# Kernel tuning notes

Hardware: AMD Instinct MI355X
Metric: run time of the kernel (lower is better)

## Reference

```python
import jax, jax.numpy as jnp
import numpy as np

NUM_WORDS = 32768
MAX_CHARS = 20
NUM_CHARS = 128
EMB = 64
H = 128   # word_hidden_size (per direction)
C = 128   # context_vector_size


def setup_inputs() -> dict:
    key = jax.random.key(0)
    ks = jax.random.split(key, 16)
    s = 1.0 / np.sqrt(H)  # torch GRU default init scale
    u = lambda k, shape, sc: jax.random.uniform(k, shape, jnp.float32, -sc, sc)
    inp = {
        'padded_char_tensor': jax.random.randint(ks[0], (NUM_WORDS, MAX_CHARS), 0, NUM_CHARS),
        'sequence_lens': jax.random.randint(ks[1], (NUM_WORDS,), 1, MAX_CHARS + 1),
        'emb': jax.random.normal(ks[2], (NUM_CHARS, EMB), jnp.float32),
        # forward-direction GRU params (torch layout: gates r,z,n stacked)
        'Wih_f': u(ks[3], (3 * H, EMB), s),
        'Whh_f': u(ks[4], (3 * H, H), s),
        'bih_f': u(ks[5], (3 * H,), s),
        'bhh_f': u(ks[6], (3 * H,), s),
        # backward-direction GRU params
        'Wih_b': u(ks[7], (3 * H, EMB), s),
        'Whh_b': u(ks[8], (3 * H, H), s),
        'bih_b': u(ks[9], (3 * H,), s),
        'bhh_b': u(ks[10], (3 * H,), s),
        # word_projection Linear(2H -> C)
        'Wp': u(ks[11], (C, 2 * H), 1.0 / np.sqrt(2 * H)),
        'bp': u(ks[12], (C,), 1.0 / np.sqrt(2 * H)),
        # word context vector [C, 1]
        'ctx': u(ks[13], (C, 1), 0.1),
    }
    return inp


def _gru_dir(x_proj, Whh, bhh):
    # x_proj: [B, T, 3H] precomputed input projection; scan over T
    Hn = Whh.shape[1]
    def step(h, xt):
        hp = h @ Whh.T + bhh
        r = jax.nn.sigmoid(xt[:, :Hn] + hp[:, :Hn])
        z = jax.nn.sigmoid(xt[:, Hn:2 * Hn] + hp[:, Hn:2 * Hn])
        n = jnp.tanh(xt[:, 2 * Hn:] + r * hp[:, 2 * Hn:])
        h = (1.0 - z) * n + z * h
        return h, h
    h0 = jnp.zeros((x_proj.shape[0], Hn), x_proj.dtype)
    _, ys = jax.lax.scan(step, h0, x_proj.transpose(1, 0, 2))
    return ys.transpose(1, 0, 2)  # [B, T, H]


def _rev_within(x, lens):
    # reverse each sequence within its valid length (packed-sequence semantics)
    T = x.shape[1]
    t = jnp.arange(T)[None, :]
    idx = jnp.where(t < lens[:, None], lens[:, None] - 1 - t, t)
    return jnp.take_along_axis(x, idx[:, :, None], axis=1)


def _forward(chars, lens, emb, Wih_f, Whh_f, bih_f, bhh_f,
             Wih_b, Whh_b, bih_b, bhh_b, Wp, bp, ctx):
    x = emb[chars]  # [B, T, EMB]; dropout_p=0 -> identity
    mask = (jnp.arange(x.shape[1])[None, :] < lens[:, None])  # [B, T]
    out_f = _gru_dir(x @ Wih_f.T + bih_f, Whh_f, bhh_f)
    xb = _rev_within(x, lens)
    out_b = _gru_dir(xb @ Wih_b.T + bih_b, Whh_b, bhh_b)
    out_b = _rev_within(out_b, lens)
    # pad_packed_sequence zero-pads beyond each length
    out = jnp.concatenate([out_f, out_b], axis=-1) * mask[:, :, None]  # [B, T, 2H]
    proj = jnp.tanh(out @ Wp.T + bp)                # [B, T, C]
    scores = jnp.einsum('btc,c->bt', proj, ctx[:, 0])
    att = jax.nn.softmax(scores, axis=-1)           # softmax over char positions
    return jnp.einsum('bt,btd->bd', att, out)       # [B, 2H]


def reference(padded_char_tensor, sequence_lens, emb, Wih_f, Whh_f, bih_f, bhh_f,
              Wih_b, Whh_b, bih_b, bhh_b, Wp, bp, ctx):
    return _forward(padded_char_tensor, sequence_lens, emb, Wih_f, Whh_f, bih_f,
                    bhh_f, Wih_b, Whh_b, bih_b, bhh_b, Wp, bp, ctx)
```

## Files before the change

### kernel.cpp

```cpp
#include <hip/hip_runtime.h>
#include <hip/hip_bf16.h>
#include <stdint.h>


typedef unsigned short u16;
typedef float f32x4 __attribute__((ext_vector_type(4)));
typedef __bf16 bf16x8 __attribute__((ext_vector_type(8)));

#if __has_builtin(__builtin_amdgcn_exp2f)
#define EXP2F(x) __builtin_amdgcn_exp2f(x)
#else
#define EXP2F(x) exp2f(x)
#endif
#if __has_builtin(__builtin_amdgcn_rcpf)
#define RCPF(x) __builtin_amdgcn_rcpf(x)
#else
#define RCPF(x) (1.0f / (x))
#endif

#define LOG2E 1.4426950408889634f

__device__ __forceinline__ u16 f2b(float f) {
  uint32_t u = __builtin_bit_cast(uint32_t, f);
  u = u + 0x7FFFu + ((u >> 16) & 1u);
  return (u16)(u >> 16);
}
__device__ __forceinline__ float b2f(u16 s) {
  uint32_t u = ((uint32_t)s) << 16;
  return __builtin_bit_cast(float, u);
}
__device__ __forceinline__ float fast_tanh(float x) {
  return 1.0f - 2.0f * RCPF(EXP2F(2.0f * LOG2E * x) + 1.0f);
}
__device__ __forceinline__ uint32_t cvtpk(float a, float b) {
  uint32_t r;
  asm("v_cvt_pk_bf16_f32 %0, %1, %2" : "=v"(r) : "v"(a), "v"(b));
  return r;
}

__global__ void prep_kernel(
    const float* __restrict__ emb,
    const float* __restrict__ wih_f, const float* __restrict__ bih_f,
    const float* __restrict__ wih_b, const float* __restrict__ bih_b,
    const float* __restrict__ bhh_f, const float* __restrict__ bhh_b,
    const float* __restrict__ whh_f_in, const float* __restrict__ whh_b_in,
    const float* __restrict__ wp_in,
    float* __restrict__ xpf_f, float* __restrict__ xpf_b,
    u16* __restrict__ whhf, u16* __restrict__ whhb, u16* __restrict__ wpf) {
  int gid = blockIdx.x * 256 + threadIdx.x;
  if (blockIdx.x < 384) {
    int e = gid;
    int d = (e >= 49152) ? 1 : 0;
    int r = e - d * 49152;
    int j = r & 3;
    int e2 = r >> 2;
    int cls = e2 % 3;
    int e3 = e2 / 3;
    int grp = e3 & 3;
    int e4 = e3 >> 2;
    int wv = e4 & 7;
    int c = e4 >> 3;
    int row = cls * 128 + wv * 16 + grp * 4 + j;
    const float* wih = d ? wih_b : wih_f;
    const float* bih = d ? bih_b : bih_f;
    const float* bhh = d ? bhh_b : bhh_f;
    const float4* e4p = (const float4*)(emb + c * 64);
    const float4* w4p = (const float4*)(wih + row * 64);
    float s = 0.f;
#pragma unroll
    for (int q = 0; q < 16; q++) {
      float4 a = e4p[q], b = w4p[q];
      s += a.x * b.x + a.y * b.y + a.z * b.z + a.w * b.w;
    }
    s += bih[row];
    float scale;
    if (cls < 2) {
      s += bhh[row];
      scale = -LOG2E;
    } else {
      scale = 2.0f * LOG2E;
    }
    (d ? xpf_b : xpf_f)[r] = s * scale;
  } else if (blockIdx.x < 432) {
    int idx = gid - 384 * 256;
    int d = (idx >= 6144) ? 1 : 0;
    int r = idx - d * 6144;
    int lane = r & 63, kt = (r >> 6) & 3, nt = r >> 8;
    float scale = (nt < 16) ? -LOG2E : 2.0f * LOG2E;
    int n = nt * 16 + (lane & 15);
    int k0 = kt * 32 + (lane >> 4) * 8;
    const float* w = d ? whh_b_in : whh_f_in;
    u16* o = (d ? whhb : whhf) + r * 8;
    for (int j = 0; j < 8; j++) o[j] = f2b(w[n * 128 + k0 + j] * scale);
  } else {
    int idx = gid - 432 * 256;
    if (idx < 4096) {
      int lane = idx & 63, kt = (idx >> 6) & 7, nt = idx >> 9;
      int n = nt * 16 + (lane & 15);
      int k0 = kt * 32 + (lane >> 4) * 8;
      u16* o = wpf + idx * 8;
      for (int j = 0; j < 8; j++) o[j] = f2b(wp_in[n * 256 + k0 + j]);
    }
  }
}

__global__ void sort_zero(int* __restrict__ bins) {
  if (threadIdx.x < 32) bins[threadIdx.x] = 0;
}
__global__ void sort_hist(const int* __restrict__ lens, int* __restrict__ bins) {
  __shared__ int hcnt[32];
  int tid = threadIdx.x;
  if (tid < 32) hcnt[tid] = 0;
  __syncthreads();
  int gid = blockIdx.x * 256 + tid;
  int l = lens[gid] & 31;
  atomicAdd(&hcnt[l], 1);
  __syncthreads();
  if (tid < 32 && hcnt[tid]) atomicAdd(&bins[tid], hcnt[tid]);
}
__global__ void sort_scan(const int* __restrict__ bins, int* __restrict__ offsw,
                          const float* __restrict__ bp,
                          const float* __restrict__ ctx,
                          float* __restrict__ c0out) {
  if (threadIdx.x == 0 && blockIdx.x == 0) {
    int off = 0;
    for (int l = 0; l < 32; l++) {
      offsw[l] = off;
      off += bins[l];
    }
    float c0 = 0.f;
    for (int c = 0; c < 128; c++) c0 += fast_tanh(bp[c]) * ctx[c];
    *c0out = c0;
  }
}
__global__ void sort_scat(const int* __restrict__ lens, int* __restrict__ offsw,
                          int* __restrict__ perm) {
  __shared__ int lcnt[32];
  __shared__ int lbase[32];
  int tid = threadIdx.x;
  if (tid < 32) lcnt[tid] = 0;
  __syncthreads();
  int gid = blockIdx.x * 256 + tid;
  int l = lens[gid] & 31;
  int lr = atomicAdd(&lcnt[l], 1);
  __syncthreads();
  if (tid < 32) lbase[tid] = lcnt[tid] ? atomicAdd(&offsw[tid], lcnt[tid]) : 0;
  __syncthreads();
  perm[lbase[l] + lr] = gid;
}

__global__ __launch_bounds__(512, 4) void gru_kernel(
    const int* __restrict__ chars, const int* __restrict__ lens,
    const int* __restrict__ perm,
    const float* __restrict__ xpf_f, const float* __restrict__ xpf_b,
    const u16* __restrict__ whhf, const u16* __restrict__ whhb,
    const float* __restrict__ bhh_f, const float* __restrict__ bhh_b,
    u16* __restrict__ hf, u16* __restrict__ hb, int word_off, int nbd) {
  const int bid = blockIdx.x;
  const int dir = bid & 1;
  const int wg = nbd - 1 - (bid >> 1);
  const int tid = threadIdx.x;

  __shared__ int perm_s[16];
  __shared__ unsigned char lens_s[16];
  __shared__ int coff_s[320];
  __shared__ u16 h_s[2][2048];

  if (tid < 16) {
    int p = perm[word_off + wg * 16 + tid];
    perm_s[tid] = p;
    lens_s[tid] = (unsigned char)lens[p];
  }
  for (int i = tid; i < 1024; i += 512) ((uint32_t*)h_s)[i] = 0u;
  __syncthreads();
  for (int i = tid; i < 320; i += 512) {
    int w = i & 15, s = i >> 4;
    int L = lens_s[w];
    int t = dir ? ((s < L) ? (L - 1 - s) : s) : s;
    coff_s[s * 16 + w] = chars[perm_s[w] * 20 + t] * 384;
  }

  const float* xp = dir ? xpf_b : xpf_f;
  const u16* whh = dir ? whhb : whhf;
  const float* bhh = dir ? bhh_b : bhh_f;
  u16* hout = (dir ? hb : hf) + (size_t)wg * 16 * 2560;

  const int wv = tid >> 6, ln = tid & 63, word = ln & 15, grp = ln >> 4;
  const float* xpt = xp + (wv * 4 + grp) * 12;

  bf16x8 Wf[3][4];
#pragma unroll
  for (int cls = 0; cls < 3; cls++) {
    int nt = cls * 8 + wv;
#pragma unroll
    for (int kt = 0; kt < 4; kt++)
      Wf[cls][kt] = *(const bf16x8*)(whh + (((nt * 4 + kt) * 64 + ln) << 3));
  }
  float4 bhn = *(const float4*)(bhh + 256 + wv * 16 + grp * 4);
  bhn.x *= 2.0f * LOG2E; bhn.y *= 2.0f * LOG2E;
  bhn.z *= 2.0f * LOG2E; bhn.w *= 2.0f * LOG2E;

  __syncthreads();

  const int Lmax = lens_s[15];

  const int hw_off =
      (((wv >> 1) * 64) + (word | (((wv & 1) * 2 + (grp >> 1)) << 4))) * 16 +
      (grp & 1) * 8;
  const int swd = tid >> 5;
  const int k4 = (tid & 31) << 2;
  const int sL = lens_s[swd];
  const int hs_off =
      (((k4 >> 5) * 64) + (swd | (((k4 >> 3) & 3) << 4))) * 16 + (k4 & 7) * 2;

  char* hsb = (char*)h_s;

  float hreg[4] = {0.f, 0.f, 0.f, 0.f};
  f32x4 xA0, xA1, xA2, xB0, xB1, xB2;
  {
    int off = coff_s[word];
    xA0 = *(const f32x4*)(xpt + off);
    xA1 = *(const f32x4*)(xpt + off + 4);
    xA2 = *(const f32x4*)(xpt + off + 8);
  }

#define GSTEP(S, PAR, XC0, XC1, XC2, XN0, XN1, XN2)                           \
  {                                                                           \
    if ((S) + 1 < Lmax) {                                                     \
      int off = coff_s[((S) + 1) * 16 + word];                                \
      XN0 = *(const f32x4*)(xpt + off);                                       \
      XN1 = *(const f32x4*)(xpt + off + 4);                                   \
      XN2 = *(const f32x4*)(xpt + off + 8);                                   \
    }                                                                         \
    f32x4 a0 = (f32x4){0.f, 0.f, 0.f, 0.f};                                   \
    f32x4 a1 = (f32x4){0.f, 0.f, 0.f, 0.f};                                   \
    f32x4 a2 = (f32x4){bhn.x, bhn.y, bhn.z, bhn.w};                           \
    _Pragma("unroll")                                                         \
    for (int kt = 0; kt < 4; kt++) {                                          \
      bf16x8 Hf =                                                             \
          *(const bf16x8*)(hsb + (PAR) * 4096 + ((kt * 64 + ln) << 4));       \
      a0 = __builtin_amdgcn_mfma_f32_16x16x32_bf16(Wf[0][kt], Hf, a0, 0, 0, 0); \
      a1 = __builtin_amdgcn_mfma_f32_16x16x32_bf16(Wf[1][kt], Hf, a1, 0, 0, 0); \
      a2 = __builtin_amdgcn_mfma_f32_16x16x32_bf16(Wf[2][kt], Hf, a2, 0, 0, 0); \
    }                                                                         \
    _Pragma("unroll")                                                         \
    for (int r = 0; r < 4; r++) {                                             \
      float rr = RCPF(1.0f + EXP2F(XC0[r] + a0[r]));                          \
      float zz = RCPF(1.0f + EXP2F(XC1[r] + a1[r]));                          \
      float na = fmaf(rr, a2[r], XC2[r]);                                     \
      float nn = fmaf(-2.0f, RCPF(EXP2F(na) + 1.0f), 1.0f);                   \
      hreg[r] = fmaf(zz, hreg[r] - nn, nn);                                   \
    }                                                                         \
    {                                                                         \
      uint2 pk = make_uint2(cvtpk(hreg[0], hreg[1]), cvtpk(hreg[2], hreg[3]));\
      *(uint2*)(hsb + ((PAR) ^ 1) * 4096 + hw_off) = pk;                      \
    }                                                                         \
    __syncthreads();                                                          \
    if ((S) < sL) {                                                           \
      int tdst = dir ? (sL - 1 - (S)) : (S);                                  \
      uint2 v = *(const uint2*)(hsb + ((PAR) ^ 1) * 4096 + hs_off);           \
      *(uint2*)(hout + ((size_t)swd * 20 + tdst) * 128 + k4) = v;             \
    }                                                                         \
  }

  for (int s = 0; s < Lmax; s += 2) {
    GSTEP(s, 0, xA0, xA1, xA2, xB0, xB1, xB2);
    if (s + 1 < Lmax) GSTEP(s + 1, 1, xB0, xB1, xB2, xA0, xA1, xA2);
  }
#undef GSTEP
}

__global__ __launch_bounds__(256, 2) void attn_kernel(
    const u16* __restrict__ hf, const u16* __restrict__ hb,
    const u16* __restrict__ wpf,
    const float* __restrict__ bp, const float* __restrict__ ctx,
    const int* __restrict__ perm, const int* __restrict__ lens,
    const float* __restrict__ c0p,
    float* __restrict__ out, int word_off) {
  const int blk = gridDim.x - 1 - blockIdx.x;
  const int lw0 = blk * 16;

  __shared__ u16 ot_s[4096];
  __shared__ float part_s[4][16];
  __shared__ int perm_s[16];
  __shared__ unsigned char lens_s[16];

  const int tid = threadIdx.x;
  const int wv = tid >> 6, ln = tid & 63, col = ln & 15, grp = ln >> 4;
  const int sw = tid >> 4;
  const int seg = tid & 15;

  if (tid < 16) {
    int p = perm[word_off + lw0 + tid];
    perm_s[tid] = p;
    lens_s[tid] = (unsigned char)lens[p];
  }
  __syncthreads();
  const int Lmax = lens_s[15];
  const int Lw = lens_s[sw];

  float bpv[2], ctxv[2];
#pragma unroll
  for (int n = 0; n < 2; n++) {
    int nt = wv + n * 4;
    bpv[n] = bp[nt * 16 + col];
    ctxv[n] = ctx[nt * 16 + col];
  }

  float facc[16];
#pragma unroll
  for (int i = 0; i < 16; i++) facc[i] = 0.f;
  float mrun = -3.0e38f, drun = 0.f;

  const u16* srcbase =
      ((seg < 8) ? hf : hb) + (size_t)(lw0 + sw) * 2560 + (seg & 7) * 16;

  uint4 vn[2];
#pragma unroll
  for (int q = 0; q < 2; q++) vn[q] = *(const uint4*)(srcbase + q * 8);

  for (int t = 0; t < Lmax; t++) {
    uint4 v[2];
    v[0] = vn[0];
    v[1] = vn[1];

#pragma unroll
    for (int q = 0; q < 2; q++) {
      int idx = seg * 2 + q;
      int kt = idx >> 2;
      int lane_a = sw | ((idx & 3) << 4);
      *(uint4*)(ot_s + ((kt * 64 + lane_a) << 3)) = v[q];
    }
    if (t + 1 < Lmax) {
      const u16* src = srcbase + (t + 1) * 128;
#pragma unroll
      for (int q = 0; q < 2; q++) vn[q] = *(const uint4*)(src + q * 8);
    }
    __syncthreads();

    f32x4 acc[2];
#pragma unroll
    for (int n = 0; n < 2; n++) acc[n] = (f32x4){bpv[n], bpv[n], bpv[n], bpv[n]};

#pragma unroll
    for (int kt = 0; kt < 8; kt++) {
      bf16x8 Af = *(const bf16x8*)(ot_s + ((kt * 64 + ln) << 3));
#pragma unroll
      for (int n = 0; n < 2; n++) {
        int nt = wv + n * 4;
        bf16x8 Bf = *(const bf16x8*)(wpf + (((nt * 8 + kt) * 64 + ln) << 3));
        acc[n] = __builtin_amdgcn_mfma_f32_16x16x32_bf16(Af, Bf, acc[n], 0, 0, 0);
      }
    }

#pragma unroll
    for (int r = 0; r < 4; r++) {
      float p = fast_tanh(acc[0][r]) * ctxv[0] + fast_tanh(acc[1][r]) * ctxv[1];
      p += __shfl_xor(p, 1, 64);
      p += __shfl_xor(p, 2, 64);
      p += __shfl_xor(p, 4, 64);
      p += __shfl_xor(p, 8, 64);
      if (col == 0) part_s[wv][grp * 4 + r] = p;
    }
    __syncthreads();

    float sc = part_s[0][sw] + part_s[1][sw] + part_s[2][sw] + part_s[3][sw];

    if (t < Lw) {
      float mnew = fmaxf(mrun, sc);
      float scale = EXP2F(LOG2E * (mrun - mnew));
      float e = EXP2F(LOG2E * (sc - mnew));
      drun = drun * scale + e;
      mrun = mnew;
#pragma unroll
      for (int q = 0; q < 2; q++) {
        const u16* pv = (const u16*)&v[q];
#pragma unroll
        for (int j = 0; j < 8; j++)
          facc[q * 8 + j] = facc[q * 8 + j] * scale + e * b2f(pv[j]);
      }
    }
  }

  drun += (float)(20 - Lw) * EXP2F(LOG2E * (*c0p - mrun));

  float inv = RCPF(drun);
  float* dst = out + (size_t)perm_s[sw] * 256 + seg * 16;
#pragma unroll
  for (int i = 0; i < 4; i++) {
    float4 o = make_float4(facc[i * 4] * inv, facc[i * 4 + 1] * inv,
                           facc[i * 4 + 2] * inv, facc[i * 4 + 3] * inv);
    *(float4*)(dst + i * 4) = o;
  }
}

extern "C" void kernel_launch(void* const* d_in, const int* in_sizes, int n_in,
                              void* d_out, int out_size, void* d_ws, size_t ws_size,
                              hipStream_t stream) {
  const int* chars = (const int*)d_in[0];
  const int* lens = (const int*)d_in[1];
  const float* emb = (const float*)d_in[2];
  const float* wih_f = (const float*)d_in[3];
  const float* whh_f = (const float*)d_in[4];
  const float* bih_f = (const float*)d_in[5];
  const float* bhh_f = (const float*)d_in[6];
  const float* wih_b = (const float*)d_in[7];
  const float* whh_b = (const float*)d_in[8];
  const float* bih_b = (const float*)d_in[9];
  const float* bhh_b = (const float*)d_in[10];
  const float* wp = (const float*)d_in[11];
  const float* bp = (const float*)d_in[12];
  const float* ctx = (const float*)d_in[13];
  float* outp = (float*)d_out;

  uint8_t* ws = (uint8_t*)d_ws;
  float* xpf_f = (float*)(ws + 0);
  float* xpf_b = (float*)(ws + 196608);
  u16* whhf = (u16*)(ws + 393216);
  u16* whhb = (u16*)(ws + 491520);
  u16* wpf = (u16*)(ws + 589824);
  int* bins = (int*)(ws + 655360);
  int* offsw = (int*)(ws + 655488);
  float* c0p = (float*)(ws + 655616);
  int* permp = (int*)(ws + 655680);
  const size_t H_OFF = 1048576;

  prep_kernel<<<448, 256, 0, stream>>>(emb, wih_f, bih_f, wih_b, bih_b, bhh_f,
                                       bhh_b, whh_f, whh_b, wp, xpf_f, xpf_b,
                                       whhf, whhb, wpf);
  sort_zero<<<1, 64, 0, stream>>>(bins);
  sort_hist<<<128, 256, 0, stream>>>(lens, bins);
  sort_scan<<<1, 64, 0, stream>>>(bins, offsw, bp, ctx, c0p);
  sort_scat<<<128, 256, 0, stream>>>(lens, offsw, permp);

  const size_t per_word = 20 * 128 * 2 * 2;
  size_t avail = (ws_size > H_OFF) ? (ws_size - H_OFF) : 0;
  int maxw = (int)(avail / per_word) & ~63;
  if (maxw > 32768) maxw = 32768;
  if (maxw < 64) maxw = 64;

  for (int done = 0; done < 32768;) {
    int nw = (32768 - done < maxw) ? (32768 - done) : maxw;
    u16* hfp = (u16*)(ws + H_OFF);
    u16* hbp = hfp + (size_t)nw * 2560;
    int nbd = nw / 16;
    gru_kernel<<<2 * nbd, 512, 0, stream>>>(chars, lens, permp, xpf_f, xpf_b,
                                            whhf, whhb, bhh_f, bhh_b, hfp, hbp,
                                            done, nbd);
    attn_kernel<<<nw / 16, 256, 0, stream>>>(hfp, hbp, wpf, bp, ctx, permp,
                                             lens, c0p, outp, done);
    done += nw;
  }
}
```

Before: 276.3 us.

## Process two 16-word groups per GRU block to interleave independent recurrences

Each GRU workgroup now handles 32 words as two independent 16-word sub-batches, issuing MFMA chains for both before the gate math so the two recurrences can hide each other's latency and share one barrier per step. Register-resident Whh weights are reused across twice as many words and the grid is halved. The cross-step prefetch of input projections is dropped in favour of loading at the start of each step. Risks include higher register pressure under the 512x4 launch bounds, fewer blocks to fill the GPU, and a loop bound set by the longest of 32 words.

```diff
diff --git a/kernel.cpp b/kernel.cpp
--- a/kernel.cpp
+++ b/kernel.cpp
@@ -161,29 +161,29 @@
   const int wg = nbd - 1 - (bid >> 1);
   const int tid = threadIdx.x;
 
-  __shared__ int perm_s[16];
-  __shared__ unsigned char lens_s[16];
-  __shared__ int coff_s[320];
-  __shared__ u16 h_s[2][2048];
-
-  if (tid < 16) {
-    int p = perm[word_off + wg * 16 + tid];
+  __shared__ int perm_s[32];
+  __shared__ unsigned char lens_s[32];
+  __shared__ int coff_s[640];
+  __shared__ u16 h_s[2][2][2048];
+
+  if (tid < 32) {
+    int p = perm[word_off + wg * 32 + tid];
     perm_s[tid] = p;
     lens_s[tid] = (unsigned char)lens[p];
   }
-  for (int i = tid; i < 1024; i += 512) ((uint32_t*)h_s)[i] = 0u;
-  __syncthreads();
-  for (int i = tid; i < 320; i += 512) {
-    int w = i & 15, s = i >> 4;
+  for (int i = tid; i < 4096; i += 512) ((uint32_t*)h_s)[i] = 0u;
+  __syncthreads();
+  for (int i = tid; i < 640; i += 512) {
+    int w = i & 31, s = i >> 5;
     int L = lens_s[w];
     int t = dir ? ((s < L) ? (L - 1 - s) : s) : s;
-    coff_s[s * 16 + w] = chars[perm_s[w] * 20 + t] * 384;
+    coff_s[s * 32 + w] = chars[perm_s[w] * 20 + t] * 384;
   }
 
   const float* xp = dir ? xpf_b : xpf_f;
   const u16* whh = dir ? whhb : whhf;
   const float* bhh = dir ? bhh_b : bhh_f;
-  u16* hout = (dir ? hb : hf) + (size_t)wg * 16 * 2560;
+  u16* hout = (dir ? hb : hf) + (size_t)wg * 32 * 2560;
 
   const int wv = tid >> 6, ln = tid & 63, word = ln & 15, grp = ln >> 4;
   const float* xpt = xp + (wv * 4 + grp) * 12;
@@ -202,36 +202,31 @@
 
   __syncthreads();
 
-  const int Lmax = lens_s[15];
+  const int Lmax = lens_s[31];
 
   const int hw_off =
       (((wv >> 1) * 64) + (word | (((wv & 1) * 2 + (grp >> 1)) << 4))) * 16 +
       (grp & 1) * 8;
   const int swd = tid >> 5;
   const int k4 = (tid & 31) << 2;
-  const int sL = lens_s[swd];
+  const int sLA = lens_s[swd];
+  const int sLB = lens_s[16 + swd];
   const int hs_off =
       (((k4 >> 5) * 64) + (swd | (((k4 >> 3) & 3) << 4))) * 16 + (k4 & 7) * 2;
+  u16* houtA = hout + (size_t)swd * 2560 + k4;
+  u16* houtB = hout + (size_t)(16 + swd) * 2560 + k4;
 
   char* hsb = (char*)h_s;
 
-  float hreg[4] = {0.f, 0.f, 0.f, 0.f};
-  f32x4 xA0, xA1, xA2, xB0, xB1, xB2;
-  {
-    int off = coff_s[word];
-    xA0 = *(const f32x4*)(xpt + off);
-    xA1 = *(const f32x4*)(xpt + off + 4);
-    xA2 = *(const f32x4*)(xpt + off + 8);
-  }
-
-#define GSTEP(S, PAR, XC0, XC1, XC2, XN0, XN1, XN2)                           \
+  float hA[4] = {0.f, 0.f, 0.f, 0.f};
+  float hB[4] = {0.f, 0.f, 0.f, 0.f};
+
+#define GSTEP(S, PAR)                                                         \
   {                                                                           \
-    if ((S) + 1 < Lmax) {                                                     \
-      int off = coff_s[((S) + 1) * 16 + word];                                \
-      XN0 = *(const f32x4*)(xpt + off);                                       \
-      XN1 = *(const f32x4*)(xpt + off + 4);                                   \
-      XN2 = *(const f32x4*)(xpt + off + 8);                                   \
-    }                                                                         \
+    int offA = coff_s[(S) * 32 + word];                                       \
+    f32x4 xA0 = *(const f32x4*)(xpt + offA);                                  \
+    f32x4 xA1 = *(const f32x4*)(xpt + offA + 4);                              \
+    f32x4 xA2 = *(const f32x4*)(xpt + offA + 8);                              \
     f32x4 a0 = (f32x4){0.f, 0.f, 0.f, 0.f};                                   \
     f32x4 a1 = (f32x4){0.f, 0.f, 0.f, 0.f};                                   \
     f32x4 a2 = (f32x4){bhn.x, bhn.y, bhn.z, bhn.w};                           \
@@ -243,29 +238,61 @@
       a1 = __builtin_amdgcn_mfma_f32_16x16x32_bf16(Wf[1][kt], Hf, a1, 0, 0, 0); \
       a2 = __builtin_amdgcn_mfma_f32_16x16x32_bf16(Wf[2][kt], Hf, a2, 0, 0, 0); \
     }                                                                         \
+    int offB = coff_s[(S) * 32 + 16 + word];                                  \
+    f32x4 xB0 = *(const f32x4*)(xpt + offB);                                  \
+    f32x4 xB1 = *(const f32x4*)(xpt + offB + 4);                              \
+    f32x4 xB2 = *(const f32x4*)(xpt + offB + 8);                              \
+    f32x4 b0 = (f32x4){0.f, 0.f, 0.f, 0.f};                                   \
+    f32x4 b1 = (f32x4){0.f, 0.f, 0.f, 0.f};                                   \
+    f32x4 b2 = (f32x4){bhn.x, bhn.y, bhn.z, bhn.w};                           \
+    _Pragma("unroll")                                                         \
+    for (int kt = 0; kt < 4; kt++) {                                          \
+      bf16x8 Hf = *(const bf16x8*)(hsb + 8192 + (PAR) * 4096 +                \
+                                   ((kt * 64 + ln) << 4));                    \
+      b0 = __builtin_amdgcn_mfma_f32_16x16x32_bf16(Wf[0][kt], Hf, b0, 0, 0, 0); \
+      b1 = __builtin_amdgcn_mfma_f32_16x16x32_bf16(Wf[1][kt], Hf, b1, 0, 0, 0); \
+      b2 = __builtin_amdgcn_mfma_f32_16x16x32_bf16(Wf[2][kt], Hf, b2, 0, 0, 0); \
+    }                                                                         \
     _Pragma("unroll")                                                         \
     for (int r = 0; r < 4; r++) {                                             \
-      float rr = RCPF(1.0f + EXP2F(XC0[r] + a0[r]));                          \
-      float zz = RCPF(1.0f + EXP2F(XC1[r] + a1[r]));                          \
-      float na = fmaf(rr, a2[r], XC2[r]);                                     \
+      float rr = RCPF(1.0f + EXP2F(xA0[r] + a0[r]));                          \
+      float zz = RCPF(1.0f + EXP2F(xA1[r] + a1[r]));                          \
+      float na = fmaf(rr, a2[r], xA2[r]);                                     \
       float nn = fmaf(-2.0f, RCPF(EXP2F(na) + 1.0f), 1.0f);                   \
-      hreg[r] = fmaf(zz, hreg[r] - nn, nn);                                   \
+      hA[r] = fmaf(zz, hA[r] - nn, nn);                                       \
     }                                                                         \
     {                                                                         \
-      uint2 pk = make_uint2(cvtpk(hreg[0], hreg[1]), cvtpk(hreg[2], hreg[3]));\
+      uint2 pk = make_uint2(cvtpk(hA[0], hA[1]), cvtpk(hA[2], hA[3]));        \
       *(uint2*)(hsb + ((PAR) ^ 1) * 4096 + hw_off) = pk;                      \
     }                                                                         \
+    _Pragma("unroll")                                                         \
+    for (int r = 0; r < 4; r++) {                                             \
+      float rr = RCPF(1.0f + EXP2F(xB0[r] + b0[r]));                          \
+      float zz = RCPF(1.0f + EXP2F(xB1[r] + b1[r]));                          \
+      float na = fmaf(rr, b2[r], xB2[r]);                                     \
+      float nn = fmaf(-2.0f, RCPF(EXP2F(na) + 1.0f), 1.0f);                   \
+      hB[r] = fmaf(zz, hB[r] - nn, nn);                                       \
+    }                                                                         \
+    {                                                                         \
+      uint2 pk = make_uint2(cvtpk(hB[0], hB[1]), cvtpk(hB[2], hB[3]));        \
+      *(uint2*)(hsb + 8192 + ((PAR) ^ 1) * 4096 + hw_off) = pk;               \
+    }                                                                         \
     __syncthreads();                                                          \
-    if ((S) < sL) {                                                           \
-      int tdst = dir ? (sL - 1 - (S)) : (S);                                  \
+    if ((S) < sLA) {                                                          \
+      int tdst = dir ? (sLA - 1 - (S)) : (S);                                 \
       uint2 v = *(const uint2*)(hsb + ((PAR) ^ 1) * 4096 + hs_off);           \
-      *(uint2*)(hout + ((size_t)swd * 20 + tdst) * 128 + k4) = v;             \
+      *(uint2*)(houtA + tdst * 128) = v;                                      \
+    }                                                                         \
+    if ((S) < sLB) {                                                          \
+      int tdst = dir ? (sLB - 1 - (S)) : (S);                                 \
+      uint2 v = *(const uint2*)(hsb + 8192 + ((PAR) ^ 1) * 4096 + hs_off);    \
+      *(uint2*)(houtB + tdst * 128) = v;                                      \
     }                                                                         \
   }
 
   for (int s = 0; s < Lmax; s += 2) {
-    GSTEP(s, 0, xA0, xA1, xA2, xB0, xB1, xB2);
-    if (s + 1 < Lmax) GSTEP(s + 1, 1, xB0, xB1, xB2, xA0, xA1, xA2);
+    GSTEP(s, 0);
+    if (s + 1 < Lmax) GSTEP(s + 1, 1);
   }
 #undef GSTEP
 }
@@ -443,7 +470,7 @@
     int nw = (32768 - done < maxw) ? (32768 - done) : maxw;
     u16* hfp = (u16*)(ws + H_OFF);
     u16* hbp = hfp + (size_t)nw * 2560;
-    int nbd = nw / 16;
+    int nbd = nw / 32;
     gru_kernel<<<2 * nbd, 512, 0, stream>>>(chars, lens, permp, xpf_f, xpf_b,
                                             whhf, whhb, bhh_f, bhh_b, hfp, hbp,
                                             done, nbd);
```

Result: slower. 286.1 us (+3.5%).

## Give each wave its own 16 words so the GRU recurrence needs no block barriers

Applied to the files above, without the earlier changes.

The GRU kernel now handles 128 words per block, and each of its 8 waves owns 16 words and computes all 384 gate columns for them. Before, the 8 waves split the hidden dimension and had to run a __syncthreads at every timestep. The full recurrent weight matrix (96 KB) is staged in shared memory and read each step, instead of being held in registers as a per-wave slice. Each wave keeps its hidden state in a private shared-memory pack buffer, which removes block-wide barriers and lets each wave stop at its own max length. The costs are heavy LDS traffic for the weights, much lower occupancy from about 128 KB of shared memory, and 8x more serial MFMA work per wave per step.

```diff
diff --git a/kernel.cpp b/kernel.cpp
--- a/kernel.cpp
+++ b/kernel.cpp
@@ -149,7 +149,7 @@
   perm[lbase[l] + lr] = gid;
 }
 
-__global__ __launch_bounds__(512, 4) void gru_kernel(
+__global__ __launch_bounds__(512, 2) void gru_nobar(
     const int* __restrict__ chars, const int* __restrict__ lens,
     const int* __restrict__ perm,
     const float* __restrict__ xpf_f, const float* __restrict__ xpf_b,
@@ -161,113 +161,101 @@
   const int wg = nbd - 1 - (bid >> 1);
   const int tid = threadIdx.x;
 
-  __shared__ int perm_s[16];
-  __shared__ unsigned char lens_s[16];
-  __shared__ int coff_s[320];
-  __shared__ u16 h_s[2][2048];
-
-  if (tid < 16) {
-    int p = perm[word_off + wg * 16 + tid];
-    perm_s[tid] = p;
-    lens_s[tid] = (unsigned char)lens[p];
-  }
-  for (int i = tid; i < 1024; i += 512) ((uint32_t*)h_s)[i] = 0u;
-  __syncthreads();
-  for (int i = tid; i < 320; i += 512) {
-    int w = i & 15, s = i >> 4;
+  __shared__ u16 whh_s[49152];
+  __shared__ u16 pack_s[8][2048];
+  __shared__ unsigned char chars_s[2560];
+  __shared__ unsigned char lens_s[128];
+
+  const u16* whh = dir ? whhb : whhf;
+  const float* xp = dir ? xpf_b : xpf_f;
+  const float* bhh = dir ? bhh_b : bhh_f;
+
+  if (tid < 128) lens_s[tid] = (unsigned char)lens[perm[word_off + wg * 128 + tid]];
+  {
+    const uint4* src = (const uint4*)whh;
+    uint4* dst = (uint4*)whh_s;
+#pragma unroll
+    for (int i = 0; i < 12; i++) dst[tid + i * 512] = src[tid + i * 512];
+  }
+  for (int i = tid; i < 8192; i += 512) ((uint32_t*)pack_s)[i] = 0u;
+  __syncthreads();
+  for (int i = tid; i < 2560; i += 512) {
+    int w = i & 127, s = i >> 7;
     int L = lens_s[w];
     int t = dir ? ((s < L) ? (L - 1 - s) : s) : s;
-    coff_s[s * 16 + w] = chars[perm_s[w] * 20 + t] * 384;
-  }
-
-  const float* xp = dir ? xpf_b : xpf_f;
-  const u16* whh = dir ? whhb : whhf;
-  const float* bhh = dir ? bhh_b : bhh_f;
-  u16* hout = (dir ? hb : hf) + (size_t)wg * 16 * 2560;
+    chars_s[s * 128 + w] = (unsigned char)chars[perm[word_off + wg * 128 + w] * 20 + t];
+  }
+  __syncthreads();
 
   const int wv = tid >> 6, ln = tid & 63, word = ln & 15, grp = ln >> 4;
-  const float* xpt = xp + (wv * 4 + grp) * 12;
-
-  bf16x8 Wf[3][4];
-#pragma unroll
-  for (int cls = 0; cls < 3; cls++) {
-    int nt = cls * 8 + wv;
+  const int wl = wv * 16 + word;
+  const int Lw = lens_s[wl];
+  const int Lmax = lens_s[wv * 16 + 15];
+
+  u16* hout = (dir ? hb : hf) + (size_t)(wg * 128 + wl) * 2560 + grp * 4;
+
+  char* pb = (char*)pack_s[wv];
+  const char* ws_ = (const char*)whh_s;
+
+  f32x4 bhn[8];
+#pragma unroll
+  for (int nt = 0; nt < 8; nt++) {
+    float4 t4 = *(const float4*)(bhh + 256 + nt * 16 + grp * 4);
+    bhn[nt] = (f32x4){t4.x * 2.0f * LOG2E, t4.y * 2.0f * LOG2E,
+                      t4.z * 2.0f * LOG2E, t4.w * 2.0f * LOG2E};
+  }
+
+  float h[8][4];
+#pragma unroll
+  for (int nt = 0; nt < 8; nt++)
+#pragma unroll
+    for (int r = 0; r < 4; r++) h[nt][r] = 0.f;
+
+  const float* xpg = xp + grp * 12;
+
+  for (int s = 0; s < Lmax; s++) {
+    bf16x8 Hf[4];
 #pragma unroll
     for (int kt = 0; kt < 4; kt++)
-      Wf[cls][kt] = *(const bf16x8*)(whh + (((nt * 4 + kt) * 64 + ln) << 3));
-  }
-  float4 bhn = *(const float4*)(bhh + 256 + wv * 16 + grp * 4);
-  bhn.x *= 2.0f * LOG2E; bhn.y *= 2.0f * LOG2E;
-  bhn.z *= 2.0f * LOG2E; bhn.w *= 2.0f * LOG2E;
-
-  __syncthreads();
-
-  const int Lmax = lens_s[15];
-
-  const int hw_off =
-      (((wv >> 1) * 64) + (word | (((wv & 1) * 2 + (grp >> 1)) << 4))) * 16 +
-      (grp & 1) * 8;
-  const int swd = tid >> 5;
-  const int k4 = (tid & 31) << 2;
-  const int sL = lens_s[swd];
-  const int hs_off =
-      (((k4 >> 5) * 64) + (swd | (((k4 >> 3) & 3) << 4))) * 16 + (k4 & 7) * 2;
-
-  char* hsb = (char*)h_s;
-
-  float hreg[4] = {0.f, 0.f, 0.f, 0.f};
-  f32x4 xA0, xA1, xA2, xB0, xB1, xB2;
-  {
-    int off = coff_s[word];
-    xA0 = *(const f32x4*)(xpt + off);
-    xA1 = *(const f32x4*)(xpt + off + 4);
-    xA2 = *(const f32x4*)(xpt + off + 8);
-  }
-
-#define GSTEP(S, PAR, XC0, XC1, XC2, XN0, XN1, XN2)                           \
-  {                                                                           \
-    if ((S) + 1 < Lmax) {                                                     \
-      int off = coff_s[((S) + 1) * 16 + word];                                \
-      XN0 = *(const f32x4*)(xpt + off);                                       \
-      XN1 = *(const f32x4*)(xpt + off + 4);                                   \
-      XN2 = *(const f32x4*)(xpt + off + 8);                                   \
-    }                                                                         \
-    f32x4 a0 = (f32x4){0.f, 0.f, 0.f, 0.f};                                   \
-    f32x4 a1 = (f32x4){0.f, 0.f, 0.f, 0.f};                                   \
-    f32x4 a2 = (f32x4){bhn.x, bhn.y, bhn.z, bhn.w};                           \
-    _Pragma("unroll")                                                         \
-    for (int kt = 0; kt < 4; kt++) {                                          \
-      bf16x8 Hf =                                                             \
-          *(const bf16x8*)(hsb + (PAR) * 4096 + ((kt * 64 + ln) << 4));       \
-      a0 = __builtin_amdgcn_mfma_f32_16x16x32_bf16(Wf[0][kt], Hf, a0, 0, 0, 0); \
-      a1 = __builtin_amdgcn_mfma_f32_16x16x32_bf16(Wf[1][kt], Hf, a1, 0, 0, 0); \
-      a2 = __builtin_amdgcn_mfma_f32_16x16x32_bf16(Wf[2][kt], Hf, a2, 0, 0, 0); \
-    }                                                                         \
-    _Pragma("unroll")                                                         \
-    for (int r = 0; r < 4; r++) {                                             \
-      float rr = RCPF(1.0f + EXP2F(XC0[r] + a0[r]));                          \
-      float zz = RCPF(1.0f + EXP2F(XC1[r] + a1[r]));                          \
-      float na = fmaf(rr, a2[r], XC2[r]);                                     \
-      float nn = fmaf(-2.0f, RCPF(EXP2F(na) + 1.0f), 1.0f);                   \
-      hreg[r] = fmaf(zz, hreg[r] - nn, nn);                                   \
-    }                                                                         \
-    {                                                                         \
-      uint2 pk = make_uint2(cvtpk(hreg[0], hreg[1]), cvtpk(hreg[2], hreg[3]));\
-      *(uint2*)(hsb + ((PAR) ^ 1) * 4096 + hw_off) = pk;                      \
-    }                                                                         \
-    __syncthreads();                                                          \
-    if ((S) < sL) {                                                           \
-      int tdst = dir ? (sL - 1 - (S)) : (S);                                  \
-      uint2 v = *(const uint2*)(hsb + ((PAR) ^ 1) * 4096 + hs_off);           \
-      *(uint2*)(hout + ((size_t)swd * 20 + tdst) * 128 + k4) = v;             \
-    }                                                                         \
-  }
-
-  for (int s = 0; s < Lmax; s += 2) {
-    GSTEP(s, 0, xA0, xA1, xA2, xB0, xB1, xB2);
-    if (s + 1 < Lmax) GSTEP(s + 1, 1, xB0, xB1, xB2, xA0, xA1, xA2);
-  }
-#undef GSTEP
+      Hf[kt] = *(const bf16x8*)(pb + ((kt * 64 + ln) << 4));
+
+    int c = chars_s[s * 128 + wl];
+    const float* xr = xpg + (c << 8) + (c << 7);
+    int t = dir ? (Lw - 1 - s) : s;
+    bool valid = (s < Lw);
+
+#pragma unroll
+    for (int nt = 0; nt < 8; nt++) {
+      f32x4 x0 = *(const f32x4*)(xr + nt * 48);
+      f32x4 x1 = *(const f32x4*)(xr + nt * 48 + 4);
+      f32x4 x2 = *(const f32x4*)(xr + nt * 48 + 8);
+      f32x4 a0 = (f32x4){0.f, 0.f, 0.f, 0.f};
+      f32x4 a1 = (f32x4){0.f, 0.f, 0.f, 0.f};
+      f32x4 a2 = bhn[nt];
+#pragma unroll
+      for (int kt = 0; kt < 4; kt++) {
+        bf16x8 A0 = *(const bf16x8*)(ws_ + ((((0 * 8 + nt) * 4 + kt) * 64 + ln) << 4));
+        a0 = __builtin_amdgcn_mfma_f32_16x16x32_bf16(A0, Hf[kt], a0, 0, 0, 0);
+        bf16x8 A1 = *(const bf16x8*)(ws_ + ((((1 * 8 + nt) * 4 + kt) * 64 + ln) << 4));
+        a1 = __builtin_amdgcn_mfma_f32_16x16x32_bf16(A1, Hf[kt], a1, 0, 0, 0);
+        bf16x8 A2 = *(const bf16x8*)(ws_ + ((((2 * 8 + nt) * 4 + kt) * 64 + ln) << 4));
+        a2 = __builtin_amdgcn_mfma_f32_16x16x32_bf16(A2, Hf[kt], a2, 0, 0, 0);
+      }
+#pragma unroll
+      for (int r = 0; r < 4; r++) {
+        float rr = RCPF(1.0f + EXP2F(x0[r] + a0[r]));
+        float zz = RCPF(1.0f + EXP2F(x1[r] + a1[r]));
+        float na = fmaf(rr, a2[r], x2[r]);
+        float nn = fmaf(-2.0f, RCPF(EXP2F(na) + 1.0f), 1.0f);
+        h[nt][r] = fmaf(zz, h[nt][r] - nn, nn);
+      }
+      uint2 pk = make_uint2(cvtpk(h[nt][0], h[nt][1]), cvtpk(h[nt][2], h[nt][3]));
+      int pw = ((((nt >> 1) << 6) + (word | (((nt & 1) * 2 + (grp >> 1)) << 4))) << 4) +
+               ((grp & 1) << 3);
+      *(uint2*)(pb + pw) = pk;
+      if (valid) *(uint2*)(hout + t * 128 + nt * 16) = pk;
+    }
+  }
 }
 
 __global__ __launch_bounds__(256, 2) void attn_kernel(
@@ -435,18 +423,18 @@
 
   const size_t per_word = 20 * 128 * 2 * 2;
   size_t avail = (ws_size > H_OFF) ? (ws_size - H_OFF) : 0;
-  int maxw = (int)(avail / per_word) & ~63;
+  int maxw = (int)(avail / per_word) & ~127;
   if (maxw > 32768) maxw = 32768;
-  if (maxw < 64) maxw = 64;
+  if (maxw < 128) maxw = 128;
 
   for (int done = 0; done < 32768;) {
     int nw = (32768 - done < maxw) ? (32768 - done) : maxw;
     u16* hfp = (u16*)(ws + H_OFF);
     u16* hbp = hfp + (size_t)nw * 2560;
-    int nbd = nw / 16;
-    gru_kernel<<<2 * nbd, 512, 0, stream>>>(chars, lens, permp, xpf_f, xpf_b,
-                                            whhf, whhb, bhh_f, bhh_b, hfp, hbp,
-                                            done, nbd);
+    int nbd = nw / 128;
+    gru_nobar<<<2 * nbd, 512, 0, stream>>>(chars, lens, permp, xpf_f, xpf_b,
+                                           whhf, whhb, bhh_f, bhh_b, hfp, hbp,
+                                           done, nbd);
     attn_kernel<<<nw / 16, 256, 0, stream>>>(hfp, hbp, wpf, bp, ctx, permp,
                                              lens, c0p, outp, done);
     done += nw;
```

New measurement: 336.8 us. 21.9% more time.
